# Kernel optimization log

Measured on AMD Instinct MI355X. Metric: run time of the kernel, lower is better.

## Reference

```python
import jax, jax.numpy as jnp
import numpy as np

N_SYS = 512      # number of crystal systems in the batch
N_ATOM = 32      # atoms per system (uniform for the reference)
N = N_SYS * N_ATOM            # 16384 total atoms
M = N_SYS * N_ATOM * N_ATOM   # 524288 dense intra-system edges
R = 16           # lattice translation points per edge
E = 128          # embed_dim
H = 8            # num_heads


def setup_inputs() -> dict:
    key = jax.random.key(0)
    ks = jax.random.split(key, 6)
    x = jax.random.normal(ks[0], (N, E), jnp.float32)
    in_proj_weight = jax.random.normal(ks[1], (3 * E, E), jnp.float32) / np.float32(np.sqrt(E))
    in_proj_bias = jnp.zeros((3 * E,), jnp.float32)
    out_proj_weight = jax.random.normal(ks[2], (E, E), jnp.float32) / np.float32(np.sqrt(E))
    out_proj_bias = jnp.zeros((E,), jnp.float32)
    # per-node per-head Gaussian exponents; must be negative for convergent lattice sums
    alpha = -(jax.random.uniform(ks[3], (N, H), jnp.float32) * 0.9 + 0.1)
    # squared distances from atom i to lattice images of atom j, up to ~5 Angstrom
    dist2 = jax.random.uniform(ks[4], (M, R), jnp.float32) * 25.0
    # dense intra-system edge list in (query-major) block order, as Crystalformer assumes
    base = (np.arange(N_SYS, dtype=np.int32) * N_ATOM)[:, None, None]
    qi = np.arange(N_ATOM, dtype=np.int32)[None, :, None]
    kj = np.arange(N_ATOM, dtype=np.int32)[None, None, :]
    e0 = np.broadcast_to(base + qi, (N_SYS, N_ATOM, N_ATOM)).reshape(-1)
    e1 = np.broadcast_to(base + kj, (N_SYS, N_ATOM, N_ATOM)).reshape(-1)
    edges = jnp.asarray(np.stack([e0, e1]), jnp.int32)
    batch = jnp.asarray(np.repeat(np.arange(N_SYS, dtype=np.int32), N_ATOM))
    return {
        "x": x,
        "in_proj_weight": in_proj_weight,
        "in_proj_bias": in_proj_bias,
        "out_proj_weight": out_proj_weight,
        "out_proj_bias": out_proj_bias,
        "alpha": alpha,
        "dist2": dist2,
        "edges": edges,
        "batch": batch,
    }


def reference(x, in_proj_weight, in_proj_bias, out_proj_weight, out_proj_bias,
              alpha, dist2, edges, batch):
    n, e = x.shape
    h = alpha.shape[1]
    dh = e // h
    # in-projection (self-attention: q = k = v = x)
    qkv = x @ in_proj_weight.T + in_proj_bias           # [N, 3E]
    q, k, v = jnp.split(qkv, 3, axis=-1)
    q = q.reshape(n, h, dh) / jnp.sqrt(jnp.asarray(dh, x.dtype))
    k = k.reshape(n, h, dh)
    v = v.reshape(n, h, dh)
    e0, e1 = edges[0], edges[1]
    # per-edge dot-product score, gathered q/k  -> [M, H]
    attn = jnp.einsum("mhd,mhd->mh", q[e0], k[e1])
    # real-domain lattice-sum attention bias: logsumexp_r(alpha_i * |r|^2)  -> [M, H]
    aw = jax.nn.logsumexp(alpha[e0][:, :, None] * dist2[:, None, :], axis=-1)
    s = attn + aw
    # segment softmax over each query's neighborhood (norm_func_mode=0 'default')
    smax = jax.ops.segment_max(s, e0, num_segments=n)   # [N, H]
    p = jnp.exp(s - smax[e0])
    denom = jax.ops.segment_sum(p, e0, num_segments=n)  # [N, H]
    p = p / denom[e0]
    # scatter-add aggregation of gathered values  -> [N, H, dh]
    out = jax.ops.segment_sum(p[:, :, None] * v[e1], e0, num_segments=n)
    # out-projection
    out = out.reshape(n, e) @ out_proj_weight.T + out_proj_bias
    return out
```

## Files before the change

### kernel.cpp

```cpp
#include <hip/hip_runtime.h>
#include <hip/hip_bf16.h>

#define LOG2E_F 1.4426950408889634f

typedef __attribute__((ext_vector_type(8))) short short8;
typedef __attribute__((ext_vector_type(4))) float f32x4;

__device__ inline unsigned short f2b(float f) {
    __hip_bfloat16 h = __float2bfloat16(f);
    return *reinterpret_cast<unsigned short*>(&h);
}

__device__ inline short8 load_frag_f32(const float* p) {
    const float4 lo = *(const float4*)p;
    const float4 hi = *(const float4*)(p + 4);
    short8 r;
    r[0] = (short)f2b(lo.x); r[1] = (short)f2b(lo.y);
    r[2] = (short)f2b(lo.z); r[3] = (short)f2b(lo.w);
    r[4] = (short)f2b(hi.x); r[5] = (short)f2b(hi.y);
    r[6] = (short)f2b(hi.z); r[7] = (short)f2b(hi.w);
    return r;
}

__global__ __launch_bounds__(512, 2) void fused2_kernel(
    const float* __restrict__ x, const float* __restrict__ Win,
    const float* __restrict__ bin, const float* __restrict__ Wout,
    const float* __restrict__ bout, const float* __restrict__ alpha,
    const float* __restrict__ dist2, float* __restrict__ out)
{
    __shared__ float qkvl[2][3][32][164];
    __shared__ unsigned short aggb[2][32][136];

    const int tid  = threadIdx.x;
    const int g    = tid >> 8;
    const int t    = tid & 255;
    const int sys  = blockIdx.x * 2 + g;
    const int lane = t & 63;
    const int wv   = t >> 6;
    const int r16  = lane & 15;
    const int kg   = lane >> 4;
    const int base = sys << 5;

    short8 af[2][4];
    #pragma unroll
    for (int rt = 0; rt < 2; ++rt)
        #pragma unroll
        for (int ks = 0; ks < 4; ++ks)
            af[rt][ks] = load_frag_f32(
                x + (size_t)(base + rt * 16 + r16) * 128 + ks * 32 + kg * 8);

    #pragma unroll
    for (int j = 0; j < 6; ++j) {
        const int ct = wv * 6 + j;
        const int c  = ct * 16 + r16;
        short8 bf[4];
        #pragma unroll
        for (int ks = 0; ks < 4; ++ks)
            bf[ks] = load_frag_f32(Win + (size_t)c * 128 + ks * 32 + kg * 8);
        const float bias_v = bin[c];
        const int   bufi   = ct >> 3;
        const int   hh     = ct & 7;
        const float scale  = (bufi == 0) ? (0.25f * LOG2E_F) : 1.0f;

        #pragma unroll
        for (int rt = 0; rt < 2; ++rt) {
            f32x4 acc = {0.f, 0.f, 0.f, 0.f};
            #pragma unroll
            for (int ks = 0; ks < 4; ++ks)
                acc = __builtin_amdgcn_mfma_f32_16x16x32_bf16(af[rt][ks], bf[ks], acc, 0, 0, 0);
            #pragma unroll
            for (int r = 0; r < 4; ++r) {
                const int atom = rt * 16 + kg * 4 + r;
                qkvl[g][bufi][atom][hh * 20 + r16] = (acc[r] + bias_v) * scale;
            }
        }
    }

    const int qi = t >> 3;
    const int h  = t & 7;
    const float al2 = alpha[(size_t)(base + qi) * 8 + h] * LOG2E_F;

    __syncthreads();

    float qreg[16];
    {
        const float* qrow = &qkvl[g][0][qi][h * 20];
        #pragma unroll
        for (int d4 = 0; d4 < 4; ++d4) {
            const float4 tq = *(const float4*)(qrow + (d4 << 2));
            qreg[d4 * 4 + 0] = tq.x; qreg[d4 * 4 + 1] = tq.y;
            qreg[d4 * 4 + 2] = tq.z; qreg[d4 * 4 + 3] = tq.w;
        }
    }

    float den = 0.f;
    float acc[16] = {};
    const float* dp = dist2 + (size_t)(sys * 1024 + qi * 32) * 16;

    #pragma unroll 4
    for (int kj = 0; kj < 32; ++kj, dp += 16) {
        const float4 t0 = *(const float4*)(dp + 0);
        const float4 t1 = *(const float4*)(dp + 4);
        const float4 t2 = *(const float4*)(dp + 8);
        const float4 t3 = *(const float4*)(dp + 12);
        const float mn = fminf(
            fminf(fminf(fminf(t0.x, t0.y), fminf(t0.z, t0.w)),
                  fminf(fminf(t1.x, t1.y), fminf(t1.z, t1.w))),
            fminf(fminf(fminf(t2.x, t2.y), fminf(t2.z, t2.w)),
                  fminf(fminf(t3.x, t3.y), fminf(t3.z, t3.w))));
        const float c0 = al2 * mn;
        float e0 = __builtin_amdgcn_exp2f(fmaf(al2, t0.x, -c0));
        e0 += __builtin_amdgcn_exp2f(fmaf(al2, t0.y, -c0));
        e0 += __builtin_amdgcn_exp2f(fmaf(al2, t0.z, -c0));
        e0 += __builtin_amdgcn_exp2f(fmaf(al2, t0.w, -c0));
        float e1 = __builtin_amdgcn_exp2f(fmaf(al2, t1.x, -c0));
        e1 += __builtin_amdgcn_exp2f(fmaf(al2, t1.y, -c0));
        e1 += __builtin_amdgcn_exp2f(fmaf(al2, t1.z, -c0));
        e1 += __builtin_amdgcn_exp2f(fmaf(al2, t1.w, -c0));
        float e2 = __builtin_amdgcn_exp2f(fmaf(al2, t2.x, -c0));
        e2 += __builtin_amdgcn_exp2f(fmaf(al2, t2.y, -c0));
        e2 += __builtin_amdgcn_exp2f(fmaf(al2, t2.z, -c0));
        e2 += __builtin_amdgcn_exp2f(fmaf(al2, t2.w, -c0));
        float e3 = __builtin_amdgcn_exp2f(fmaf(al2, t3.x, -c0));
        e3 += __builtin_amdgcn_exp2f(fmaf(al2, t3.y, -c0));
        e3 += __builtin_amdgcn_exp2f(fmaf(al2, t3.z, -c0));
        e3 += __builtin_amdgcn_exp2f(fmaf(al2, t3.w, -c0));
        const float ssum = (e0 + e1) + (e2 + e3);

        const float* kr = &qkvl[g][1][kj][h * 20];
        const float4 k0 = *(const float4*)(kr + 0);
        const float4 k1 = *(const float4*)(kr + 4);
        const float4 k2 = *(const float4*)(kr + 8);
        const float4 k3 = *(const float4*)(kr + 12);
        float p0 = qreg[0] * k0.x, p1 = qreg[1] * k0.y;
        float p2 = qreg[2] * k0.z, p3 = qreg[3] * k0.w;
        p0 = fmaf(qreg[4],  k1.x, p0); p1 = fmaf(qreg[5],  k1.y, p1);
        p2 = fmaf(qreg[6],  k1.z, p2); p3 = fmaf(qreg[7],  k1.w, p3);
        p0 = fmaf(qreg[8],  k2.x, p0); p1 = fmaf(qreg[9],  k2.y, p1);
        p2 = fmaf(qreg[10], k2.z, p2); p3 = fmaf(qreg[11], k2.w, p3);
        p0 = fmaf(qreg[12], k3.x, p0); p1 = fmaf(qreg[13], k3.y, p1);
        p2 = fmaf(qreg[14], k3.z, p2); p3 = fmaf(qreg[15], k3.w, p3);
        const float dot = (p0 + p1) + (p2 + p3);

        const float b = dot + c0;
        const float p = __builtin_amdgcn_exp2f(b - 16.0f) * ssum;
        den += p;

        const float* vr = &qkvl[g][2][kj][h * 20];
        const float4 v0 = *(const float4*)(vr + 0);
        const float4 v1 = *(const float4*)(vr + 4);
        const float4 v2 = *(const float4*)(vr + 8);
        const float4 v3 = *(const float4*)(vr + 12);
        acc[0]  = fmaf(p, v0.x, acc[0]);  acc[1]  = fmaf(p, v0.y, acc[1]);
        acc[2]  = fmaf(p, v0.z, acc[2]);  acc[3]  = fmaf(p, v0.w, acc[3]);
        acc[4]  = fmaf(p, v1.x, acc[4]);  acc[5]  = fmaf(p, v1.y, acc[5]);
        acc[6]  = fmaf(p, v1.z, acc[6]);  acc[7]  = fmaf(p, v1.w, acc[7]);
        acc[8]  = fmaf(p, v2.x, acc[8]);  acc[9]  = fmaf(p, v2.y, acc[9]);
        acc[10] = fmaf(p, v2.z, acc[10]); acc[11] = fmaf(p, v2.w, acc[11]);
        acc[12] = fmaf(p, v3.x, acc[12]); acc[13] = fmaf(p, v3.y, acc[13]);
        acc[14] = fmaf(p, v3.z, acc[14]); acc[15] = fmaf(p, v3.w, acc[15]);
    }

    {
        const float inv = 1.0f / den;
        unsigned short* op = &aggb[g][qi][h * 16];
        uint4 o0, o1;
        o0.x = (unsigned)f2b(acc[0]  * inv) | ((unsigned)f2b(acc[1]  * inv) << 16);
        o0.y = (unsigned)f2b(acc[2]  * inv) | ((unsigned)f2b(acc[3]  * inv) << 16);
        o0.z = (unsigned)f2b(acc[4]  * inv) | ((unsigned)f2b(acc[5]  * inv) << 16);
        o0.w = (unsigned)f2b(acc[6]  * inv) | ((unsigned)f2b(acc[7]  * inv) << 16);
        o1.x = (unsigned)f2b(acc[8]  * inv) | ((unsigned)f2b(acc[9]  * inv) << 16);
        o1.y = (unsigned)f2b(acc[10] * inv) | ((unsigned)f2b(acc[11] * inv) << 16);
        o1.z = (unsigned)f2b(acc[12] * inv) | ((unsigned)f2b(acc[13] * inv) << 16);
        o1.w = (unsigned)f2b(acc[14] * inv) | ((unsigned)f2b(acc[15] * inv) << 16);
        *(uint4*)op       = o0;
        *(uint4*)(op + 8) = o1;
    }

    __syncthreads();

    short8 aA[2][4];
    #pragma unroll
    for (int rt = 0; rt < 2; ++rt)
        #pragma unroll
        for (int ks = 0; ks < 4; ++ks)
            aA[rt][ks] = *(const short8*)(&aggb[g][rt * 16 + r16][ks * 32 + kg * 8]);

    #pragma unroll
    for (int j = 0; j < 2; ++j) {
        const int ct = wv * 2 + j;
        const int c  = ct * 16 + r16;
        short8 bf[4];
        #pragma unroll
        for (int ks = 0; ks < 4; ++ks)
            bf[ks] = load_frag_f32(Wout + (size_t)c * 128 + ks * 32 + kg * 8);
        const float bias_v = bout[c];
        #pragma unroll
        for (int rt = 0; rt < 2; ++rt) {
            f32x4 oacc = {0.f, 0.f, 0.f, 0.f};
            #pragma unroll
            for (int ks = 0; ks < 4; ++ks)
                oacc = __builtin_amdgcn_mfma_f32_16x16x32_bf16(aA[rt][ks], bf[ks], oacc, 0, 0, 0);
            #pragma unroll
            for (int r = 0; r < 4; ++r) {
                const int row = base + rt * 16 + kg * 4 + r;
                out[(size_t)row * 128 + c] = oacc[r] + bias_v;
            }
        }
    }
}

extern "C" void kernel_launch(void* const* d_in, const int* in_sizes, int n_in,
                              void* d_out, int out_size, void* d_ws, size_t ws_size,
                              hipStream_t stream)
{
    const float* x     = (const float*)d_in[0];
    const float* Win   = (const float*)d_in[1];
    const float* bin   = (const float*)d_in[2];
    const float* Wout  = (const float*)d_in[3];
    const float* bout  = (const float*)d_in[4];
    const float* alpha = (const float*)d_in[5];
    const float* dist2 = (const float*)d_in[6];

    fused2_kernel<<<dim3(256), 512, 0, stream>>>(
        x, Win, bin, Wout, bout, alpha, dist2, (float*)d_out);
}
```

Baseline: 39.98 us.

## Pre-convert inputs to bf16 in a prep kernel and use packed f32 math

Adds a separate prep kernel that converts x, Win and Wout to bf16 in workspace memory, so the fused kernel loads ready-made bf16 fragments and skips the per-fragment conversions. The inner lattice-sum and attention loop is also rewritten with two-wide float vectors so the compiler can emit packed FMA, min and mul instructions. The trade-off is an extra launch plus a write and re-read of x through global memory. Every block also re-converts the shared weights, and that work is what gets saved.

New measurement: 35.92 us. 10.2% less time.

```diff
diff --git a/kernel.cpp b/kernel.cpp
--- a/kernel.cpp
+++ b/kernel.cpp
@@ -5,6 +5,7 @@
 
 typedef __attribute__((ext_vector_type(8))) short short8;
 typedef __attribute__((ext_vector_type(4))) float f32x4;
+typedef __attribute__((ext_vector_type(2))) float f32x2;
 
 __device__ inline unsigned short f2b(float f) {
     __hip_bfloat16 h = __float2bfloat16(f);
@@ -22,9 +23,28 @@
     return r;
 }
 
+__device__ inline f32x2 mk2(float a, float b) { f32x2 r; r.x = a; r.y = b; return r; }
+#define PK_FMA(a, b, c) __builtin_elementwise_fma((a), (b), (c))
+#define PK_MIN(a, b)    __builtin_elementwise_min((a), (b))
+
+__global__ __launch_bounds__(256) void prep_kernel(
+    const float* __restrict__ x, const float* __restrict__ Win,
+    const float* __restrict__ Wout,
+    unsigned short* __restrict__ xbf, unsigned short* __restrict__ winbf,
+    unsigned short* __restrict__ woutbf)
+{
+    const int i = blockIdx.x * 256 + threadIdx.x;
+    const float* src; unsigned short* dst; size_t off;
+    if (i < 262144)       { src = x;    dst = xbf;    off = (size_t)i * 8; }
+    else if (i < 268288)  { src = Win;  dst = winbf;  off = (size_t)(i - 262144) * 8; }
+    else                  { src = Wout; dst = woutbf; off = (size_t)(i - 268288) * 8; }
+    const short8 r = load_frag_f32(src + off);
+    *(short8*)(dst + off) = r;
+}
+
 __global__ __launch_bounds__(512, 2) void fused2_kernel(
-    const float* __restrict__ x, const float* __restrict__ Win,
-    const float* __restrict__ bin, const float* __restrict__ Wout,
+    const unsigned short* __restrict__ xbf, const unsigned short* __restrict__ winbf,
+    const float* __restrict__ bin, const unsigned short* __restrict__ woutbf,
     const float* __restrict__ bout, const float* __restrict__ alpha,
     const float* __restrict__ dist2, float* __restrict__ out)
 {
@@ -46,8 +66,8 @@
     for (int rt = 0; rt < 2; ++rt)
         #pragma unroll
         for (int ks = 0; ks < 4; ++ks)
-            af[rt][ks] = load_frag_f32(
-                x + (size_t)(base + rt * 16 + r16) * 128 + ks * 32 + kg * 8);
+            af[rt][ks] = *(const short8*)(
+                xbf + (size_t)(base + rt * 16 + r16) * 128 + ks * 32 + kg * 8);
 
     #pragma unroll
     for (int j = 0; j < 6; ++j) {
@@ -56,7 +76,7 @@
         short8 bf[4];
         #pragma unroll
         for (int ks = 0; ks < 4; ++ks)
-            bf[ks] = load_frag_f32(Win + (size_t)c * 128 + ks * 32 + kg * 8);
+            bf[ks] = *(const short8*)(winbf + (size_t)c * 128 + ks * 32 + kg * 8);
         const float bias_v = bin[c];
         const int   bufi   = ct >> 3;
         const int   hh     = ct & 7;
@@ -79,22 +99,23 @@
     const int qi = t >> 3;
     const int h  = t & 7;
     const float al2 = alpha[(size_t)(base + qi) * 8 + h] * LOG2E_F;
+    const f32x2 al22 = mk2(al2, al2);
 
     __syncthreads();
 
-    float qreg[16];
+    f32x2 q2[8];
     {
         const float* qrow = &qkvl[g][0][qi][h * 20];
         #pragma unroll
         for (int d4 = 0; d4 < 4; ++d4) {
             const float4 tq = *(const float4*)(qrow + (d4 << 2));
-            qreg[d4 * 4 + 0] = tq.x; qreg[d4 * 4 + 1] = tq.y;
-            qreg[d4 * 4 + 2] = tq.z; qreg[d4 * 4 + 3] = tq.w;
+            q2[d4 * 2 + 0] = mk2(tq.x, tq.y);
+            q2[d4 * 2 + 1] = mk2(tq.z, tq.w);
         }
     }
 
     float den = 0.f;
-    float acc[16] = {};
+    f32x2 acc2[8] = {};
     const float* dp = dist2 + (size_t)(sys * 1024 + qi * 32) * 16;
 
     #pragma unroll 4
@@ -103,76 +124,76 @@
         const float4 t1 = *(const float4*)(dp + 4);
         const float4 t2 = *(const float4*)(dp + 8);
         const float4 t3 = *(const float4*)(dp + 12);
-        const float mn = fminf(
-            fminf(fminf(fminf(t0.x, t0.y), fminf(t0.z, t0.w)),
-                  fminf(fminf(t1.x, t1.y), fminf(t1.z, t1.w))),
-            fminf(fminf(fminf(t2.x, t2.y), fminf(t2.z, t2.w)),
-                  fminf(fminf(t3.x, t3.y), fminf(t3.z, t3.w))));
-        const float c0 = al2 * mn;
-        float e0 = __builtin_amdgcn_exp2f(fmaf(al2, t0.x, -c0));
-        e0 += __builtin_amdgcn_exp2f(fmaf(al2, t0.y, -c0));
-        e0 += __builtin_amdgcn_exp2f(fmaf(al2, t0.z, -c0));
-        e0 += __builtin_amdgcn_exp2f(fmaf(al2, t0.w, -c0));
-        float e1 = __builtin_amdgcn_exp2f(fmaf(al2, t1.x, -c0));
-        e1 += __builtin_amdgcn_exp2f(fmaf(al2, t1.y, -c0));
-        e1 += __builtin_amdgcn_exp2f(fmaf(al2, t1.z, -c0));
-        e1 += __builtin_amdgcn_exp2f(fmaf(al2, t1.w, -c0));
-        float e2 = __builtin_amdgcn_exp2f(fmaf(al2, t2.x, -c0));
-        e2 += __builtin_amdgcn_exp2f(fmaf(al2, t2.y, -c0));
-        e2 += __builtin_amdgcn_exp2f(fmaf(al2, t2.z, -c0));
-        e2 += __builtin_amdgcn_exp2f(fmaf(al2, t2.w, -c0));
-        float e3 = __builtin_amdgcn_exp2f(fmaf(al2, t3.x, -c0));
-        e3 += __builtin_amdgcn_exp2f(fmaf(al2, t3.y, -c0));
-        e3 += __builtin_amdgcn_exp2f(fmaf(al2, t3.z, -c0));
-        e3 += __builtin_amdgcn_exp2f(fmaf(al2, t3.w, -c0));
-        const float ssum = (e0 + e1) + (e2 + e3);
+        const f32x2 d2p[8] = {mk2(t0.x,t0.y), mk2(t0.z,t0.w), mk2(t1.x,t1.y), mk2(t1.z,t1.w),
+                              mk2(t2.x,t2.y), mk2(t2.z,t2.w), mk2(t3.x,t3.y), mk2(t3.z,t3.w)};
+        f32x2 mnA = PK_MIN(PK_MIN(d2p[0], d2p[1]), PK_MIN(d2p[2], d2p[3]));
+        f32x2 mnB = PK_MIN(PK_MIN(d2p[4], d2p[5]), PK_MIN(d2p[6], d2p[7]));
+        const f32x2 mn2 = PK_MIN(mnA, mnB);
+        const float mn  = fminf(mn2.x, mn2.y);
+        const float c0  = al2 * mn;
+        const f32x2 nc02 = mk2(-c0, -c0);
+
+        f32x2 ex[8];
+        #pragma unroll
+        for (int i = 0; i < 8; ++i) ex[i] = PK_FMA(al22, d2p[i], nc02);
+        f32x2 es = mk2(__builtin_amdgcn_exp2f(ex[0].x), __builtin_amdgcn_exp2f(ex[0].y));
+        #pragma unroll
+        for (int i = 1; i < 8; ++i)
+            es += mk2(__builtin_amdgcn_exp2f(ex[i].x), __builtin_amdgcn_exp2f(ex[i].y));
+        const float ssum = es.x + es.y;
 
         const float* kr = &qkvl[g][1][kj][h * 20];
         const float4 k0 = *(const float4*)(kr + 0);
         const float4 k1 = *(const float4*)(kr + 4);
         const float4 k2 = *(const float4*)(kr + 8);
         const float4 k3 = *(const float4*)(kr + 12);
-        float p0 = qreg[0] * k0.x, p1 = qreg[1] * k0.y;
-        float p2 = qreg[2] * k0.z, p3 = qreg[3] * k0.w;
-        p0 = fmaf(qreg[4],  k1.x, p0); p1 = fmaf(qreg[5],  k1.y, p1);
-        p2 = fmaf(qreg[6],  k1.z, p2); p3 = fmaf(qreg[7],  k1.w, p3);
-        p0 = fmaf(qreg[8],  k2.x, p0); p1 = fmaf(qreg[9],  k2.y, p1);
-        p2 = fmaf(qreg[10], k2.z, p2); p3 = fmaf(qreg[11], k2.w, p3);
-        p0 = fmaf(qreg[12], k3.x, p0); p1 = fmaf(qreg[13], k3.y, p1);
-        p2 = fmaf(qreg[14], k3.z, p2); p3 = fmaf(qreg[15], k3.w, p3);
-        const float dot = (p0 + p1) + (p2 + p3);
+        f32x2 dA = q2[0] * mk2(k0.x, k0.y);
+        f32x2 dB = q2[1] * mk2(k0.z, k0.w);
+        dA = PK_FMA(q2[2], mk2(k1.x, k1.y), dA);
+        dB = PK_FMA(q2[3], mk2(k1.z, k1.w), dB);
+        dA = PK_FMA(q2[4], mk2(k2.x, k2.y), dA);
+        dB = PK_FMA(q2[5], mk2(k2.z, k2.w), dB);
+        dA = PK_FMA(q2[6], mk2(k3.x, k3.y), dA);
+        dB = PK_FMA(q2[7], mk2(k3.z, k3.w), dB);
+        const float dot = (dA.x + dA.y) + (dB.x + dB.y);
 
         const float b = dot + c0;
         const float p = __builtin_amdgcn_exp2f(b - 16.0f) * ssum;
         den += p;
+        const f32x2 p2 = mk2(p, p);
 
         const float* vr = &qkvl[g][2][kj][h * 20];
         const float4 v0 = *(const float4*)(vr + 0);
         const float4 v1 = *(const float4*)(vr + 4);
         const float4 v2 = *(const float4*)(vr + 8);
         const float4 v3 = *(const float4*)(vr + 12);
-        acc[0]  = fmaf(p, v0.x, acc[0]);  acc[1]  = fmaf(p, v0.y, acc[1]);
-        acc[2]  = fmaf(p, v0.z, acc[2]);  acc[3]  = fmaf(p, v0.w, acc[3]);
-        acc[4]  = fmaf(p, v1.x, acc[4]);  acc[5]  = fmaf(p, v1.y, acc[5]);
-        acc[6]  = fmaf(p, v1.z, acc[6]);  acc[7]  = fmaf(p, v1.w, acc[7]);
-        acc[8]  = fmaf(p, v2.x, acc[8]);  acc[9]  = fmaf(p, v2.y, acc[9]);
-        acc[10] = fmaf(p, v2.z, acc[10]); acc[11] = fmaf(p, v2.w, acc[11]);
-        acc[12] = fmaf(p, v3.x, acc[12]); acc[13] = fmaf(p, v3.y, acc[13]);
-        acc[14] = fmaf(p, v3.z, acc[14]); acc[15] = fmaf(p, v3.w, acc[15]);
+        acc2[0] = PK_FMA(p2, mk2(v0.x, v0.y), acc2[0]);
+        acc2[1] = PK_FMA(p2, mk2(v0.z, v0.w), acc2[1]);
+        acc2[2] = PK_FMA(p2, mk2(v1.x, v1.y), acc2[2]);
+        acc2[3] = PK_FMA(p2, mk2(v1.z, v1.w), acc2[3]);
+        acc2[4] = PK_FMA(p2, mk2(v2.x, v2.y), acc2[4]);
+        acc2[5] = PK_FMA(p2, mk2(v2.z, v2.w), acc2[5]);
+        acc2[6] = PK_FMA(p2, mk2(v3.x, v3.y), acc2[6]);
+        acc2[7] = PK_FMA(p2, mk2(v3.z, v3.w), acc2[7]);
     }
 
     {
         const float inv = 1.0f / den;
+        const f32x2 inv2 = mk2(inv, inv);
         unsigned short* op = &aggb[g][qi][h * 16];
         uint4 o0, o1;
-        o0.x = (unsigned)f2b(acc[0]  * inv) | ((unsigned)f2b(acc[1]  * inv) << 16);
-        o0.y = (unsigned)f2b(acc[2]  * inv) | ((unsigned)f2b(acc[3]  * inv) << 16);
-        o0.z = (unsigned)f2b(acc[4]  * inv) | ((unsigned)f2b(acc[5]  * inv) << 16);
-        o0.w = (unsigned)f2b(acc[6]  * inv) | ((unsigned)f2b(acc[7]  * inv) << 16);
-        o1.x = (unsigned)f2b(acc[8]  * inv) | ((unsigned)f2b(acc[9]  * inv) << 16);
-        o1.y = (unsigned)f2b(acc[10] * inv) | ((unsigned)f2b(acc[11] * inv) << 16);
-        o1.z = (unsigned)f2b(acc[12] * inv) | ((unsigned)f2b(acc[13] * inv) << 16);
-        o1.w = (unsigned)f2b(acc[14] * inv) | ((unsigned)f2b(acc[15] * inv) << 16);
+        f32x2 r0 = acc2[0] * inv2, r1 = acc2[1] * inv2;
+        f32x2 r2 = acc2[2] * inv2, r3 = acc2[3] * inv2;
+        f32x2 r4 = acc2[4] * inv2, r5 = acc2[5] * inv2;
+        f32x2 r6 = acc2[6] * inv2, r7 = acc2[7] * inv2;
+        o0.x = (unsigned)f2b(r0.x) | ((unsigned)f2b(r0.y) << 16);
+        o0.y = (unsigned)f2b(r1.x) | ((unsigned)f2b(r1.y) << 16);
+        o0.z = (unsigned)f2b(r2.x) | ((unsigned)f2b(r2.y) << 16);
+        o0.w = (unsigned)f2b(r3.x) | ((unsigned)f2b(r3.y) << 16);
+        o1.x = (unsigned)f2b(r4.x) | ((unsigned)f2b(r4.y) << 16);
+        o1.y = (unsigned)f2b(r5.x) | ((unsigned)f2b(r5.y) << 16);
+        o1.z = (unsigned)f2b(r6.x) | ((unsigned)f2b(r6.y) << 16);
+        o1.w = (unsigned)f2b(r7.x) | ((unsigned)f2b(r7.y) << 16);
         *(uint4*)op       = o0;
         *(uint4*)(op + 8) = o1;
     }
@@ -193,7 +214,7 @@
         short8 bf[4];
         #pragma unroll
         for (int ks = 0; ks < 4; ++ks)
-            bf[ks] = load_frag_f32(Wout + (size_t)c * 128 + ks * 32 + kg * 8);
+            bf[ks] = *(const short8*)(woutbf + (size_t)c * 128 + ks * 32 + kg * 8);
         const float bias_v = bout[c];
         #pragma unroll
         for (int rt = 0; rt < 2; ++rt) {
@@ -222,6 +243,11 @@
     const float* alpha = (const float*)d_in[5];
     const float* dist2 = (const float*)d_in[6];
 
+    unsigned short* xbf    = (unsigned short*)d_ws;
+    unsigned short* winbf  = xbf + (size_t)16384 * 128;
+    unsigned short* woutbf = winbf + (size_t)384 * 128;
+
+    prep_kernel<<<dim3(1056), 256, 0, stream>>>(x, Win, Wout, xbf, winbf, woutbf);
     fused2_kernel<<<dim3(256), 512, 0, stream>>>(
-        x, Win, bin, Wout, bout, alpha, dist2, (float*)d_out);
-}
+        xbf, winbf, bin, woutbf, bout, alpha, dist2, (float*)d_out);
+}
```
